# Kernel optimization log

Measured on AMD Instinct MI355X. Metric: run time of the kernel, lower is better.

The kernel has to match this reference:

```python
import jax, jax.numpy as jnp
import numpy as np

N_NODES = 30000
N_EDGES = 300000
N_TRIP = 200000
NUM_RELS = 8
F_RAW = 128
D = 256  # rgcn_in_dim == h_dim


def setup_inputs() -> dict:
    key = jax.random.key(0)
    ks = jax.random.split(key, 14)
    feats = jax.random.normal(ks[0], (N_NODES, F_RAW), jnp.float32)
    src = jax.random.randint(ks[1], (N_EDGES,), 0, N_NODES)
    dst = jax.random.randint(ks[2], (N_EDGES,), 0, N_NODES)
    etype = jax.random.randint(ks[3], (N_EDGES,), 0, NUM_RELS)
    trip_s = jax.random.randint(ks[4], (N_TRIP,), 0, N_NODES)
    trip_r = jax.random.randint(ks[5], (N_TRIP,), 0, NUM_RELS)
    trip_o = jax.random.randint(ks[6], (N_TRIP,), 0, N_NODES)
    # learned parameters
    W_affine = jax.random.normal(ks[7], (F_RAW, D), jnp.float32) * (1.0 / np.sqrt(F_RAW))
    b_affine = jnp.zeros((D,), jnp.float32)
    W_fwd = jax.random.normal(ks[8], (NUM_RELS, D, D), jnp.float32) * (1.0 / np.sqrt(D))
    W_bwd = jax.random.normal(ks[9], (NUM_RELS, D, D), jnp.float32) * (1.0 / np.sqrt(D))
    W_loop = jax.random.normal(ks[10], (D, D), jnp.float32) * (1.0 / np.sqrt(D))
    w_relation = jax.random.normal(ks[11], (NUM_RELS, D), jnp.float32)  # nn.init.normal_(0,1)
    return {
        "feats": feats, "W_affine": W_affine, "b_affine": b_affine,
        "W_fwd": W_fwd, "W_bwd": W_bwd, "W_loop": W_loop,
        "w_relation": w_relation,
        "src": src, "dst": dst, "etype": etype,
        "trip_s": trip_s, "trip_r": trip_r, "trip_o": trip_o,
    }


def reference(feats, W_affine, b_affine, W_fwd, W_bwd, W_loop, w_relation,
              src, dst, etype, trip_s, trip_r, trip_o):
    # LinearAffine: raw features -> rgcn_in_dim
    x = feats @ W_affine + b_affine                      # [N, D]
    n = x.shape[0]
    # Per-relation transforms of all node features: [R, N, D]
    tf = jnp.einsum('ni,rio->rno', x, W_fwd)
    tb = jnp.einsum('ni,rio->rno', x, W_bwd)
    # Forward-direction messages: gather per-edge transformed src, scatter-add to dst
    msg_f = tf[etype, src]                               # [E, D]
    agg = jnp.zeros((n, x.shape[1]), x.dtype).at[dst].add(msg_f)
    # Backward-direction messages: transformed dst features scattered to src
    msg_b = tb[etype, dst]                               # [E, D]
    agg = agg.at[src].add(msg_b)
    # Self-loop
    h = agg + x @ W_loop                                 # [N, D]
    # DistMult triplet scoring
    s = h[trip_s]
    r = w_relation[trip_r]
    o = h[trip_o]
    weights = jnp.sum(s * r * o, axis=1)                 # [T]
    return weights, h
```

## Files before the change

### kernel.cpp

```cpp
#include <hip/hip_runtime.h>

#define N_NODES 30000
#define N_EDGES 300000
#define N_TRIP 200000
#define NUM_RELS 8
#define F_RAW 128
#define DDIM 256

#define NBUCK (2 * NUM_RELS * N_NODES)
#define SCAN_CHUNK 1024
#define NCHUNK ((NBUCK + SCAN_CHUNK - 1) / SCAN_CHUNK)
#define NPAD (NCHUNK * SCAN_CHUNK)

#define KBIG 2304
#define KBWD 2048

typedef __attribute__((ext_vector_type(8))) short short8;
typedef __attribute__((ext_vector_type(8))) unsigned short u16x8;
typedef __attribute__((ext_vector_type(4))) float f32x4;

__device__ inline unsigned short f2bf(float f) {
  unsigned u = __builtin_bit_cast(unsigned, f);
  u = (u + 0x7FFFu + ((u >> 16) & 1u)) >> 16;
  return (unsigned short)u;
}
__device__ inline float bf2f(unsigned short s) {
  unsigned u = ((unsigned)s) << 16;
  return __builtin_bit_cast(float, u);
}

__global__ void zero_int_kernel(int* __restrict__ p, int n) {
  int i = blockIdx.x * blockDim.x + threadIdx.x;
  if (i < n) p[i] = 0;
}

__global__ void hist_kernel(const int* __restrict__ src,
                            const int* __restrict__ dst,
                            const int* __restrict__ et, int* __restrict__ cnt) {
  int e = blockIdx.x * blockDim.x + threadIdx.x;
  if (e >= N_EDGES) return;
  int r = et[e];
  atomicAdd(&cnt[r * N_NODES + dst[e]], 1);
  atomicAdd(&cnt[(NUM_RELS + r) * N_NODES + src[e]], 1);
}

__global__ __launch_bounds__(256) void scan1_kernel(const int* __restrict__ cnt,
                                                    int* __restrict__ offs,
                                                    int* __restrict__ bsum) {
  __shared__ int s[256];
  const int b = blockIdx.x, t = threadIdx.x;
  const int base = b * SCAN_CHUNK + t * 4;
  int4 v = *reinterpret_cast<const int4*>(&cnt[base]);
  int tsum = v.x + v.y + v.z + v.w;
  s[t] = tsum;
  __syncthreads();
  for (int off = 1; off < 256; off <<= 1) {
    int x = (t >= off) ? s[t - off] : 0;
    __syncthreads();
    s[t] += x;
    __syncthreads();
  }
  int excl = s[t] - tsum;
  offs[base + 0] = excl;
  offs[base + 1] = excl + v.x;
  offs[base + 2] = excl + v.x + v.y;
  offs[base + 3] = excl + v.x + v.y + v.z;
  if (t == 0) bsum[b] = s[255];
}

__global__ __launch_bounds__(512) void scan2_kernel(int* __restrict__ bsum) {
  __shared__ int s[512];
  const int t = threadIdx.x;
  int v = (t < NCHUNK) ? bsum[t] : 0;
  s[t] = v;
  __syncthreads();
  for (int off = 1; off < 512; off <<= 1) {
    int x = (t >= off) ? s[t - off] : 0;
    __syncthreads();
    s[t] += x;
    __syncthreads();
  }
  if (t < NCHUNK) bsum[t] = s[t] - v;
}

__global__ void scan3_kernel(int* __restrict__ offs,
                             const int* __restrict__ bsum,
                             int* __restrict__ cur) {
  int i = blockIdx.x * blockDim.x + threadIdx.x;
  if (i >= NPAD) return;
  int v = offs[i] + bsum[i / SCAN_CHUNK];
  offs[i] = v;
  if (i < NBUCK) cur[i] = v;
}

__global__ void fill_kernel(const int* __restrict__ src,
                            const int* __restrict__ dst,
                            const int* __restrict__ et, int* __restrict__ cur,
                            int* __restrict__ gidx) {
  int e = blockIdx.x * blockDim.x + threadIdx.x;
  if (e >= N_EDGES) return;
  int r = et[e];
  int s = src[e], d = dst[e];
  int p1 = atomicAdd(&cur[r * N_NODES + d], 1);
  gidx[p1] = s;
  int p2 = atomicAdd(&cur[(NUM_RELS + r) * N_NODES + s], 1);
  gidx[p2] = d;
}

__global__ void convert_bf16_kernel(const float* __restrict__ src,
                                    unsigned short* __restrict__ dst,
                                    int total) {
  const int i = blockIdx.x * blockDim.x + threadIdx.x;
  if (i < total) dst[i] = f2bf(src[i]);
}

__global__ void transpose_bf16_kernel(const float* __restrict__ src,
                                      unsigned short* __restrict__ dst,
                                      int R, int K, int N) {
  const int i = blockIdx.x * blockDim.x + threadIdx.x;
  const int total = R * K * N;
  if (i >= total) return;
  const int r = i / (K * N);
  const int rem = i - r * K * N;
  const int k = rem / N;
  const int n = rem - k * N;
  dst[(size_t)r * K * N + (size_t)n * K + k] = f2bf(src[i]);
}

__global__ void build_wcat2_kernel(const float* __restrict__ W8,
                                   const float* __restrict__ Wextra,
                                   unsigned short* __restrict__ dst, int KK) {
  const int i = blockIdx.x * blockDim.x + threadIdx.x;
  if (i >= 256 * KK) return;
  const int n = i / KK;
  const int kk = i - n * KK;
  float v;
  if (kk < 2048) {
    const int r = kk >> 8, k = kk & 255;
    v = W8[((size_t)r * 256 + k) * 256 + n];
  } else {
    v = Wextra[(size_t)(kk - 2048) * 256 + n];
  }
  dst[i] = f2bf(v);
}

__global__ __launch_bounds__(256) void gemm128_kernel(
    const unsigned short* __restrict__ A, int lda, int K,
    const unsigned short* __restrict__ Bt, const float* __restrict__ bias,
    unsigned short* __restrict__ Cb, int ldc, int M) {
  __shared__ __align__(16) unsigned short As[128 * 64];
  __shared__ __align__(16) unsigned short Bs[128 * 64];

  const int tid = threadIdx.x;
  const int lane = tid & 63;
  const int wave = tid >> 6;
  const int bm = blockIdx.y * 128;
  const int bn = blockIdx.x * 128;
  const int wr = wave >> 1;
  const int wc = wave & 1;
  const int g = lane >> 4;
  const int rl = lane & 15;

  f32x4 acc[4][4];
#pragma unroll
  for (int i = 0; i < 4; ++i)
#pragma unroll
    for (int j = 0; j < 4; ++j) acc[i][j] = (f32x4){0.f, 0.f, 0.f, 0.f};

  for (int k0 = 0; k0 < K; k0 += 64) {
#pragma unroll
    for (int c = 0; c < 8; ++c) {
      const int chunk = c * 4 + wave;
      if (chunk < 16) {
        const int S = chunk * 64 + lane;
        const int row = S >> 3;
        const int s = S & 7;
        int grow = bm + row;
        if (grow > M - 1) grow = M - 1;
        const int kcol = k0 + ((s ^ (row & 7)) << 3);
        const unsigned short* gp = A + (size_t)grow * lda + kcol;
        unsigned short* lp = As + (size_t)chunk * 512;
        __builtin_amdgcn_global_load_lds(
            (const __attribute__((address_space(1))) void*)gp,
            (__attribute__((address_space(3))) void*)lp, 16, 0, 0);
      } else {
        const int S = (chunk - 16) * 64 + lane;
        const int row = S >> 3;
        const int s = S & 7;
        const int kcol = k0 + ((s ^ (row & 7)) << 3);
        const unsigned short* gp = Bt + (size_t)(bn + row) * K + kcol;
        unsigned short* lp = Bs + (size_t)(chunk - 16) * 512;
        __builtin_amdgcn_global_load_lds(
            (const __attribute__((address_space(1))) void*)gp,
            (__attribute__((address_space(3))) void*)lp, 16, 0, 0);
      }
    }
    __syncthreads();

#pragma unroll
    for (int kk = 0; kk < 2; ++kk) {
      short8 a[4], b[4];
#pragma unroll
      for (int mi = 0; mi < 4; ++mi) {
        const int row = wr * 64 + mi * 16 + rl;
        const int slot = (kk * 4 + g) ^ (row & 7);
        a[mi] = *(const short8*)&As[row * 64 + slot * 8];
      }
#pragma unroll
      for (int ni = 0; ni < 4; ++ni) {
        const int row = wc * 64 + ni * 16 + rl;
        const int slot = (kk * 4 + g) ^ (row & 7);
        b[ni] = *(const short8*)&Bs[row * 64 + slot * 8];
      }
#pragma unroll
      for (int mi = 0; mi < 4; ++mi)
#pragma unroll
        for (int ni = 0; ni < 4; ++ni)
          acc[mi][ni] = __builtin_amdgcn_mfma_f32_16x16x32_bf16(
              a[mi], b[ni], acc[mi][ni], 0, 0, 0);
    }
    __syncthreads();
  }

#pragma unroll
  for (int mi = 0; mi < 4; ++mi) {
#pragma unroll
    for (int j = 0; j < 4; ++j) {
      const int row = bm + wr * 64 + mi * 16 + g * 4 + j;
      if (row >= M) continue;
#pragma unroll
      for (int ni = 0; ni < 4; ++ni) {
        const int col = bn + wc * 64 + ni * 16 + rl;
        Cb[(size_t)row * ldc + col] = f2bf(acc[mi][ni][j] + bias[col]);
      }
    }
  }
}

template <int OUT_MODE>
__global__ __launch_bounds__(256) void gemm64_kernel(
    const unsigned short* __restrict__ A, int lda, int K,
    const unsigned short* __restrict__ Bt, float* __restrict__ Cf,
    unsigned short* __restrict__ Cb, int ldc, int M, int nblk) {
  __shared__ __align__(16) unsigned short As[64 * 64];
  __shared__ __align__(16) unsigned short Bs[128 * 64];

  const int tid = threadIdx.x;
  const int lane = tid & 63;
  const int wave = tid >> 6;

  const int orig = blockIdx.x;
  const int q = nblk >> 3, r = nblk & 7;
  const int xcd = orig & 7, off = orig >> 3;
  const int wg =
      (xcd < r) ? xcd * (q + 1) + off : r * (q + 1) + (xcd - r) * q + off;
  const int bm = (wg >> 1) * 64;
  const int bn = (wg & 1) * 128;

  const int wr = wave >> 1;
  const int wc = wave & 1;
  const int g = lane >> 4;
  const int rl = lane & 15;

  f32x4 acc[2][4];
#pragma unroll
  for (int i = 0; i < 2; ++i)
#pragma unroll
    for (int j = 0; j < 4; ++j) acc[i][j] = (f32x4){0.f, 0.f, 0.f, 0.f};

  for (int k0 = 0; k0 < K; k0 += 64) {
#pragma unroll
    for (int c = 0; c < 6; ++c) {
      const int chunk = c * 4 + wave;
      if (chunk < 8) {
        const int S = chunk * 64 + lane;
        const int row = S >> 3;
        const int s = S & 7;
        int grow = bm + row;
        if (grow > M - 1) grow = M - 1;
        const unsigned short* gp =
            A + (size_t)grow * lda + k0 + ((s ^ (row & 7)) << 3);
        unsigned short* lp = As + (size_t)chunk * 512;
        __builtin_amdgcn_global_load_lds(
            (const __attribute__((address_space(1))) void*)gp,
            (__attribute__((address_space(3))) void*)lp, 16, 0, 0);
      } else {
        const int S = (chunk - 8) * 64 + lane;
        const int row = S >> 3;
        const int s = S & 7;
        const unsigned short* gp =
            Bt + (size_t)(bn + row) * K + k0 + ((s ^ (row & 7)) << 3);
        unsigned short* lp = Bs + (size_t)(chunk - 8) * 512;
        __builtin_amdgcn_global_load_lds(
            (const __attribute__((address_space(1))) void*)gp,
            (__attribute__((address_space(3))) void*)lp, 16, 0, 0);
      }
    }
    __syncthreads();

#pragma unroll
    for (int kk = 0; kk < 2; ++kk) {
      short8 a[2], b[4];
#pragma unroll
      for (int mi = 0; mi < 2; ++mi) {
        const int row = wr * 32 + mi * 16 + rl;
        const int slot = (kk * 4 + g) ^ (row & 7);
        a[mi] = *(const short8*)&As[row * 64 + slot * 8];
      }
#pragma unroll
      for (int ni = 0; ni < 4; ++ni) {
        const int row = wc * 64 + ni * 16 + rl;
        const int slot = (kk * 4 + g) ^ (row & 7);
        b[ni] = *(const short8*)&Bs[row * 64 + slot * 8];
      }
#pragma unroll
      for (int mi = 0; mi < 2; ++mi)
#pragma unroll
        for (int ni = 0; ni < 4; ++ni)
          acc[mi][ni] = __builtin_amdgcn_mfma_f32_16x16x32_bf16(
              a[mi], b[ni], acc[mi][ni], 0, 0, 0);
    }
    __syncthreads();
  }

#pragma unroll
  for (int mi = 0; mi < 2; ++mi) {
#pragma unroll
    for (int j = 0; j < 4; ++j) {
      const int row = bm + wr * 32 + mi * 16 + g * 4 + j;
      if (row >= M) continue;
#pragma unroll
      for (int ni = 0; ni < 4; ++ni) {
        const int col = bn + wc * 64 + ni * 16 + rl;
        float v = acc[mi][ni][j];
        const size_t idx = (size_t)row * ldc + col;
        if (OUT_MODE == 0) {
          Cf[idx] = v;
        } else {
          v += Cf[idx];
          Cf[idx] = v;
          Cb[idx] = f2bf(v);
        }
      }
    }
  }
}

__global__ __launch_bounds__(256) void zgatherw_kernel(
    unsigned short* __restrict__ Z, int colbase,
    const int* __restrict__ offs_base, const int* __restrict__ gidx) {
  const int lane = threadIdx.x & 63;
  const int hl = lane >> 5;
  const int l5 = lane & 31;
  const int b = blockIdx.x * 8 + (threadIdx.x >> 6) * 2 + hl;
  if (b >= NUM_RELS * N_NODES) return;
  const int r = b / N_NODES;
  const int v = b - r * N_NODES;
  const int s = offs_base[b], e = offs_base[b + 1];

  float acc[8] = {};
  for (int i = s; i < e; i += 4) {
    int g4[4];
    u16x8 xs[4];
#pragma unroll
    for (int q = 0; q < 4; ++q)
      if (i + q < e) g4[q] = gidx[i + q];
#pragma unroll
    for (int q = 0; q < 4; ++q)
      if (i + q < e)
        xs[q] = *(const u16x8*)&Z[(size_t)g4[q] * KBIG + 2048 + l5 * 8];
#pragma unroll
    for (int q = 0; q < 4; ++q)
      if (i + q < e) {
#pragma unroll
        for (int j = 0; j < 8; ++j) acc[j] += bf2f((unsigned short)xs[q][j]);
      }
  }
  u16x8 o;
#pragma unroll
  for (int j = 0; j < 8; ++j) o[j] = (short)f2bf(acc[j]);
  *(u16x8*)&Z[(size_t)v * KBIG + colbase + r * 256 + l5 * 8] = o;
}

__global__ __launch_bounds__(256) void score32_kernel(
    const unsigned short* __restrict__ hb, const float* __restrict__ wrel,
    const int* __restrict__ ts, const int* __restrict__ tr,
    const int* __restrict__ to, float* __restrict__ out, int T) {
  const int t = blockIdx.x * 8 + (threadIdx.x >> 5);
  if (t >= T) return;
  const int l5 = threadIdx.x & 31;
  const int s = ts[t];
  const int r = tr[t];
  const int o = to[t];
  const u16x8 hs = *(const u16x8*)&hb[(size_t)s * DDIM + l5 * 8];
  const u16x8 ho = *(const u16x8*)&hb[(size_t)o * DDIM + l5 * 8];
  const float4 w0 = *(const float4*)&wrel[(size_t)r * DDIM + l5 * 8];
  const float4 w1 = *(const float4*)&wrel[(size_t)r * DDIM + l5 * 8 + 4];
  float sum = bf2f((unsigned short)hs[0]) * w0.x * bf2f((unsigned short)ho[0]) +
              bf2f((unsigned short)hs[1]) * w0.y * bf2f((unsigned short)ho[1]) +
              bf2f((unsigned short)hs[2]) * w0.z * bf2f((unsigned short)ho[2]) +
              bf2f((unsigned short)hs[3]) * w0.w * bf2f((unsigned short)ho[3]) +
              bf2f((unsigned short)hs[4]) * w1.x * bf2f((unsigned short)ho[4]) +
              bf2f((unsigned short)hs[5]) * w1.y * bf2f((unsigned short)ho[5]) +
              bf2f((unsigned short)hs[6]) * w1.z * bf2f((unsigned short)ho[6]) +
              bf2f((unsigned short)hs[7]) * w1.w * bf2f((unsigned short)ho[7]);
#pragma unroll
  for (int off = 16; off; off >>= 1) sum += __shfl_down(sum, off, 32);
  if (l5 == 0) out[t] = sum;
}

extern "C" void kernel_launch(void* const* d_in, const int* in_sizes, int n_in,
                              void* d_out, int out_size, void* d_ws,
                              size_t ws_size, hipStream_t stream) {
  const float* feats = (const float*)d_in[0];
  const float* W_affine = (const float*)d_in[1];
  const float* b_affine = (const float*)d_in[2];
  const float* W_fwd = (const float*)d_in[3];
  const float* W_bwd = (const float*)d_in[4];
  const float* W_loop = (const float*)d_in[5];
  const float* w_relation = (const float*)d_in[6];
  const int* src = (const int*)d_in[7];
  const int* dst = (const int*)d_in[8];
  const int* etype = (const int*)d_in[9];
  const int* trip_s = (const int*)d_in[10];
  const int* trip_r = (const int*)d_in[11];
  const int* trip_o = (const int*)d_in[12];

  float* out_w = (float*)d_out;
  float* h = out_w + N_TRIP;

  char* ws = (char*)d_ws;
  unsigned short* fb = (unsigned short*)(ws);
  unsigned short* Z = (unsigned short*)(ws + 7680000);
  unsigned short* hbf = (unsigned short*)(ws + 145920000);
  unsigned short* Wta = (unsigned short*)(ws + 161280000);
  unsigned short* Wcat1 = (unsigned short*)(ws + 161345536);
  unsigned short* Wcat2 = (unsigned short*)(ws + 162525184);
  int* cnt = (int*)(ws + 163573760);
  int* offs = (int*)(ws + 165494784);
  int* cur = (int*)(ws + 167415808);
  int* bsum = (int*)(ws + 169336832);
  int* gidx = (int*)(ws + 169338880);

  zero_int_kernel<<<(NPAD + 255) / 256, 256, 0, stream>>>(cnt, NPAD);
  hist_kernel<<<(N_EDGES + 255) / 256, 256, 0, stream>>>(src, dst, etype, cnt);
  scan1_kernel<<<NCHUNK, 256, 0, stream>>>(cnt, offs, bsum);
  scan2_kernel<<<1, 512, 0, stream>>>(bsum);
  scan3_kernel<<<(NPAD + 255) / 256, 256, 0, stream>>>(offs, bsum, cur);
  fill_kernel<<<(N_EDGES + 255) / 256, 256, 0, stream>>>(src, dst, etype, cur,
                                                         gidx);

  convert_bf16_kernel<<<(N_NODES * F_RAW + 255) / 256, 256, 0, stream>>>(
      feats, fb, N_NODES * F_RAW);
  transpose_bf16_kernel<<<(F_RAW * DDIM + 255) / 256, 256, 0, stream>>>(
      W_affine, Wta, 1, F_RAW, DDIM);
  build_wcat2_kernel<<<(256 * KBIG + 255) / 256, 256, 0, stream>>>(
      W_fwd, W_loop, Wcat1, KBIG);
  build_wcat2_kernel<<<(256 * KBWD + 255) / 256, 256, 0, stream>>>(
      W_bwd, nullptr, Wcat2, KBWD);

  const dim3 agrid(2, (N_NODES + 127) / 128);
  gemm128_kernel<<<agrid, 256, 0, stream>>>(fb, F_RAW, F_RAW, Wta, b_affine,
                                            Z + 2048, KBIG, N_NODES);

  const int nblk = 2 * ((N_NODES + 63) / 64);
  const int zgrid = (NUM_RELS * N_NODES + 7) / 8;

  zgatherw_kernel<<<zgrid, 256, 0, stream>>>(Z, 0, offs, gidx);
  gemm64_kernel<0><<<nblk, 256, 0, stream>>>(Z, KBIG, KBIG, Wcat1, h, nullptr,
                                             DDIM, N_NODES, nblk);
  zgatherw_kernel<<<zgrid, 256, 0, stream>>>(Z, 0, offs + NUM_RELS * N_NODES,
                                             gidx);
  gemm64_kernel<2><<<nblk, 256, 0, stream>>>(Z, KBIG, KBWD, Wcat2, h, hbf,
                                             DDIM, N_NODES, nblk);

  score32_kernel<<<(N_TRIP + 7) / 8, 256, 0, stream>>>(
      hbf, w_relation, trip_s, trip_r, trip_o, out_w, N_TRIP);
}
```

Before: 298.1 us.

## Merge fwd/bwd GEMMs into one K=4352 pass with indirect sparse row pointers

Replaces the two dense Z-buffer gathers and two GEMMs with a single gather that only materialises bucket sums for buckets with two or more edges. Empty buckets point to a shared zero row and single-edge buckets point straight at the node's x row. One GEMM over the concatenated forward, backward and loop weights then reads A rows through a rowptr indirection. This removes the large dense Z writes and the read-modify-write of h between the two GEMMs. In exchange it adds a rowptr pass with an atomic slot counter and per-load indirect addressing in the GEMM A tile loads.

```diff
diff --git a/kernel.cpp b/kernel.cpp
--- a/kernel.cpp
+++ b/kernel.cpp
@@ -12,8 +12,10 @@
 #define NCHUNK ((NBUCK + SCAN_CHUNK - 1) / SCAN_CHUNK)
 #define NPAD (NCHUNK * SCAN_CHUNK)
 
-#define KBIG 2304
-#define KBWD 2048
+#define KMRG 4352
+#define ZM_ROWS 240000
+#define XB_ROW0 240000
+#define ZERO_ROW 270000
 
 typedef __attribute__((ext_vector_type(8))) short short8;
 typedef __attribute__((ext_vector_type(8))) unsigned short u16x8;
@@ -85,8 +87,11 @@
 
 __global__ void scan3_kernel(int* __restrict__ offs,
                              const int* __restrict__ bsum,
-                             int* __restrict__ cur) {
+                             int* __restrict__ cur, int* __restrict__ zrow,
+                             int* __restrict__ ctr) {
   int i = blockIdx.x * blockDim.x + threadIdx.x;
+  if (i < 128) zrow[i] = 0;
+  if (i == 0) *ctr = 0;
   if (i >= NPAD) return;
   int v = offs[i] + bsum[i / SCAN_CHUNK];
   offs[i] = v;
@@ -107,6 +112,24 @@
   gidx[p2] = d;
 }
 
+__global__ void rowptr_kernel(const int* __restrict__ offs,
+                              const int* __restrict__ gidx,
+                              int* __restrict__ rowptr, int* __restrict__ ctr) {
+  int b = blockIdx.x * blockDim.x + threadIdx.x;
+  if (b >= NBUCK) return;
+  int s = offs[b], e = offs[b + 1];
+  int cnt = e - s;
+  int rid;
+  if (cnt == 0) rid = ZERO_ROW;
+  else if (cnt == 1) rid = XB_ROW0 + gidx[s];
+  else {
+    int slot = atomicAdd(ctr, 1);
+    if (slot > ZM_ROWS - 1) slot = ZM_ROWS - 1;
+    rid = slot;
+  }
+  rowptr[b] = rid;
+}
+
 __global__ void convert_bf16_kernel(const float* __restrict__ src,
                                     unsigned short* __restrict__ dst,
                                     int total) {
@@ -127,19 +150,23 @@
   dst[(size_t)r * K * N + (size_t)n * K + k] = f2bf(src[i]);
 }
 
-__global__ void build_wcat2_kernel(const float* __restrict__ W8,
-                                   const float* __restrict__ Wextra,
-                                   unsigned short* __restrict__ dst, int KK) {
+__global__ void build_wcat3_kernel(const float* __restrict__ Wf,
+                                   const float* __restrict__ Wb,
+                                   const float* __restrict__ Wl,
+                                   unsigned short* __restrict__ dst) {
   const int i = blockIdx.x * blockDim.x + threadIdx.x;
-  if (i >= 256 * KK) return;
-  const int n = i / KK;
-  const int kk = i - n * KK;
+  if (i >= 256 * KMRG) return;
+  const int n = i / KMRG;
+  const int kk = i - n * KMRG;
   float v;
   if (kk < 2048) {
     const int r = kk >> 8, k = kk & 255;
-    v = W8[((size_t)r * 256 + k) * 256 + n];
+    v = Wf[((size_t)r * 256 + k) * 256 + n];
+  } else if (kk < 4096) {
+    const int r = (kk - 2048) >> 8, k = kk & 255;
+    v = Wb[((size_t)r * 256 + k) * 256 + n];
   } else {
-    v = Wextra[(size_t)(kk - 2048) * 256 + n];
+    v = Wl[(size_t)(kk - 4096) * 256 + n];
   }
   dst[i] = f2bf(v);
 }
@@ -237,11 +264,46 @@
   }
 }
 
-template <int OUT_MODE>
-__global__ __launch_bounds__(256) void gemm64_kernel(
-    const unsigned short* __restrict__ A, int lda, int K,
-    const unsigned short* __restrict__ Bt, float* __restrict__ Cf,
-    unsigned short* __restrict__ Cb, int ldc, int M, int nblk) {
+__global__ __launch_bounds__(256) void zgatherm_kernel(
+    unsigned short* __restrict__ rowbase, const unsigned short* __restrict__ xb,
+    const int* __restrict__ offs, const int* __restrict__ gidx,
+    const int* __restrict__ rowptr) {
+  const int lane = threadIdx.x & 63;
+  const int hl = lane >> 5;
+  const int l5 = lane & 31;
+  const int b = blockIdx.x * 8 + (threadIdx.x >> 6) * 2 + hl;
+  if (b >= NBUCK) return;
+  const int s = offs[b], e = offs[b + 1];
+  if (e - s < 2) return;
+
+  float acc[8] = {};
+  for (int i = s; i < e; i += 4) {
+    int g4[4];
+    u16x8 xs[4];
+#pragma unroll
+    for (int q = 0; q < 4; ++q)
+      if (i + q < e) g4[q] = gidx[i + q];
+#pragma unroll
+    for (int q = 0; q < 4; ++q)
+      if (i + q < e)
+        xs[q] = *(const u16x8*)&xb[(size_t)g4[q] * DDIM + l5 * 8];
+#pragma unroll
+    for (int q = 0; q < 4; ++q)
+      if (i + q < e) {
+#pragma unroll
+        for (int j = 0; j < 8; ++j) acc[j] += bf2f((unsigned short)xs[q][j]);
+      }
+  }
+  u16x8 o;
+#pragma unroll
+  for (int j = 0; j < 8; ++j) o[j] = (short)f2bf(acc[j]);
+  *(u16x8*)&rowbase[(size_t)rowptr[b] * DDIM + l5 * 8] = o;
+}
+
+__global__ __launch_bounds__(256) void gemmv_kernel(
+    const unsigned short* __restrict__ rowbase,
+    const int* __restrict__ rowptr, const unsigned short* __restrict__ Bt,
+    float* __restrict__ Cf, unsigned short* __restrict__ Cb, int M, int nblk) {
   __shared__ __align__(16) unsigned short As[64 * 64];
   __shared__ __align__(16) unsigned short Bs[128 * 64];
 
@@ -268,7 +330,9 @@
 #pragma unroll
     for (int j = 0; j < 4; ++j) acc[i][j] = (f32x4){0.f, 0.f, 0.f, 0.f};
 
-  for (int k0 = 0; k0 < K; k0 += 64) {
+  for (int k0 = 0; k0 < KMRG; k0 += 64) {
+    const int kb = k0 >> 8;
+    const int koff = k0 & 255;
 #pragma unroll
     for (int c = 0; c < 6; ++c) {
       const int chunk = c * 4 + wave;
@@ -276,10 +340,12 @@
         const int S = chunk * 64 + lane;
         const int row = S >> 3;
         const int s = S & 7;
-        int grow = bm + row;
-        if (grow > M - 1) grow = M - 1;
+        int node = bm + row;
+        if (node > M - 1) node = M - 1;
+        const int rid =
+            (kb < 16) ? rowptr[kb * N_NODES + node] : (XB_ROW0 + node);
         const unsigned short* gp =
-            A + (size_t)grow * lda + k0 + ((s ^ (row & 7)) << 3);
+            rowbase + (size_t)rid * 256 + koff + ((s ^ (row & 7)) << 3);
         unsigned short* lp = As + (size_t)chunk * 512;
         __builtin_amdgcn_global_load_lds(
             (const __attribute__((address_space(1))) void*)gp,
@@ -289,7 +355,7 @@
         const int row = S >> 3;
         const int s = S & 7;
         const unsigned short* gp =
-            Bt + (size_t)(bn + row) * K + k0 + ((s ^ (row & 7)) << 3);
+            Bt + (size_t)(bn + row) * KMRG + k0 + ((s ^ (row & 7)) << 3);
         unsigned short* lp = Bs + (size_t)(chunk - 8) * 512;
         __builtin_amdgcn_global_load_lds(
             (const __attribute__((address_space(1))) void*)gp,
@@ -332,54 +398,13 @@
 #pragma unroll
       for (int ni = 0; ni < 4; ++ni) {
         const int col = bn + wc * 64 + ni * 16 + rl;
-        float v = acc[mi][ni][j];
-        const size_t idx = (size_t)row * ldc + col;
-        if (OUT_MODE == 0) {
-          Cf[idx] = v;
-        } else {
-          v += Cf[idx];
-          Cf[idx] = v;
-          Cb[idx] = f2bf(v);
-        }
+        const float v = acc[mi][ni][j];
+        const size_t idx = (size_t)row * DDIM + col;
+        Cf[idx] = v;
+        Cb[idx] = f2bf(v);
       }
     }
   }
-}
-
-__global__ __launch_bounds__(256) void zgatherw_kernel(
-    unsigned short* __restrict__ Z, int colbase,
-    const int* __restrict__ offs_base, const int* __restrict__ gidx) {
-  const int lane = threadIdx.x & 63;
-  const int hl = lane >> 5;
-  const int l5 = lane & 31;
-  const int b = blockIdx.x * 8 + (threadIdx.x >> 6) * 2 + hl;
-  if (b >= NUM_RELS * N_NODES) return;
-  const int r = b / N_NODES;
-  const int v = b - r * N_NODES;
-  const int s = offs_base[b], e = offs_base[b + 1];
-
-  float acc[8] = {};
-  for (int i = s; i < e; i += 4) {
-    int g4[4];
-    u16x8 xs[4];
-#pragma unroll
-    for (int q = 0; q < 4; ++q)
-      if (i + q < e) g4[q] = gidx[i + q];
-#pragma unroll
-    for (int q = 0; q < 4; ++q)
-      if (i + q < e)
-        xs[q] = *(const u16x8*)&Z[(size_t)g4[q] * KBIG + 2048 + l5 * 8];
-#pragma unroll
-    for (int q = 0; q < 4; ++q)
-      if (i + q < e) {
-#pragma unroll
-        for (int j = 0; j < 8; ++j) acc[j] += bf2f((unsigned short)xs[q][j]);
-      }
-  }
-  u16x8 o;
-#pragma unroll
-  for (int j = 0; j < 8; ++j) o[j] = (short)f2bf(acc[j]);
-  *(u16x8*)&Z[(size_t)v * KBIG + colbase + r * 256 + l5 * 8] = o;
 }
 
 __global__ __launch_bounds__(256) void score32_kernel(
@@ -430,49 +455,49 @@
   float* h = out_w + N_TRIP;
 
   char* ws = (char*)d_ws;
-  unsigned short* fb = (unsigned short*)(ws);
-  unsigned short* Z = (unsigned short*)(ws + 7680000);
-  unsigned short* hbf = (unsigned short*)(ws + 145920000);
-  unsigned short* Wta = (unsigned short*)(ws + 161280000);
-  unsigned short* Wcat1 = (unsigned short*)(ws + 161345536);
-  unsigned short* Wcat2 = (unsigned short*)(ws + 162525184);
-  int* cnt = (int*)(ws + 163573760);
-  int* offs = (int*)(ws + 165494784);
-  int* cur = (int*)(ws + 167415808);
-  int* bsum = (int*)(ws + 169336832);
-  int* gidx = (int*)(ws + 169338880);
-
-  zero_int_kernel<<<(NPAD + 255) / 256, 256, 0, stream>>>(cnt, NPAD);
-  hist_kernel<<<(N_EDGES + 255) / 256, 256, 0, stream>>>(src, dst, etype, cnt);
-  scan1_kernel<<<NCHUNK, 256, 0, stream>>>(cnt, offs, bsum);
+  unsigned short* rowbase = (unsigned short*)ws;
+  unsigned short* fb = (unsigned short*)ws;
+  unsigned short* xb = (unsigned short*)(ws + 122880000);
+  int* zrow = (int*)(ws + 138240000);
+  unsigned short* hbf = (unsigned short*)(ws + 138240512);
+  int* offs = (int*)(ws + 153600512);
+  int* cntcur = (int*)(ws + 155522048);
+  int* bsum = (int*)(ws + 157443072);
+  int* gidx = (int*)(ws + 157445120);
+  int* rowptr = (int*)(ws + 159845120);
+  unsigned short* Wta = (unsigned short*)(ws + 161765120);
+  unsigned short* Wcat = (unsigned short*)(ws + 161830656);
+  int* ctr = (int*)(ws + 164058880);
+
+  zero_int_kernel<<<(NPAD + 255) / 256, 256, 0, stream>>>(cntcur, NPAD);
+  hist_kernel<<<(N_EDGES + 255) / 256, 256, 0, stream>>>(src, dst, etype,
+                                                         cntcur);
+  scan1_kernel<<<NCHUNK, 256, 0, stream>>>(cntcur, offs, bsum);
   scan2_kernel<<<1, 512, 0, stream>>>(bsum);
-  scan3_kernel<<<(NPAD + 255) / 256, 256, 0, stream>>>(offs, bsum, cur);
-  fill_kernel<<<(N_EDGES + 255) / 256, 256, 0, stream>>>(src, dst, etype, cur,
-                                                         gidx);
+  scan3_kernel<<<(NPAD + 255) / 256, 256, 0, stream>>>(offs, bsum, cntcur,
+                                                       zrow, ctr);
+  fill_kernel<<<(N_EDGES + 255) / 256, 256, 0, stream>>>(src, dst, etype,
+                                                         cntcur, gidx);
+  rowptr_kernel<<<(NBUCK + 255) / 256, 256, 0, stream>>>(offs, gidx, rowptr,
+                                                         ctr);
 
   convert_bf16_kernel<<<(N_NODES * F_RAW + 255) / 256, 256, 0, stream>>>(
       feats, fb, N_NODES * F_RAW);
   transpose_bf16_kernel<<<(F_RAW * DDIM + 255) / 256, 256, 0, stream>>>(
       W_affine, Wta, 1, F_RAW, DDIM);
-  build_wcat2_kernel<<<(256 * KBIG + 255) / 256, 256, 0, stream>>>(
-      W_fwd, W_loop, Wcat1, KBIG);
-  build_wcat2_kernel<<<(256 * KBWD + 255) / 256, 256, 0, stream>>>(
-      W_bwd, nullptr, Wcat2, KBWD);
+  build_wcat3_kernel<<<(256 * KMRG + 255) / 256, 256, 0, stream>>>(
+      W_fwd, W_bwd, W_loop, Wcat);
 
   const dim3 agrid(2, (N_NODES + 127) / 128);
   gemm128_kernel<<<agrid, 256, 0, stream>>>(fb, F_RAW, F_RAW, Wta, b_affine,
-                                            Z + 2048, KBIG, N_NODES);
+                                            xb, DDIM, N_NODES);
+
+  zgatherm_kernel<<<(NBUCK + 7) / 8, 256, 0, stream>>>(rowbase, xb, offs, gidx,
+                                                       rowptr);
 
   const int nblk = 2 * ((N_NODES + 63) / 64);
-  const int zgrid = (NUM_RELS * N_NODES + 7) / 8;
-
-  zgatherw_kernel<<<zgrid, 256, 0, stream>>>(Z, 0, offs, gidx);
-  gemm64_kernel<0><<<nblk, 256, 0, stream>>>(Z, KBIG, KBIG, Wcat1, h, nullptr,
-                                             DDIM, N_NODES, nblk);
-  zgatherw_kernel<<<zgrid, 256, 0, stream>>>(Z, 0, offs + NUM_RELS * N_NODES,
-                                             gidx);
-  gemm64_kernel<2><<<nblk, 256, 0, stream>>>(Z, KBIG, KBWD, Wcat2, h, hbf,
-                                             DDIM, N_NODES, nblk);
+  gemmv_kernel<<<nblk, 256, 0, stream>>>(rowbase, rowptr, Wcat, h, hbf,
+                                         N_NODES, nblk);
 
   score32_kernel<<<(N_TRIP + 7) / 8, 256, 0, stream>>>(
       hbf, w_relation, trip_s, trip_r, trip_o, out_w, N_TRIP);
```

Result: slower. 379.8 us (+27.4%).

## Split-K the relation GEMMs in two with atomic float accumulation

Applied to the files above, without the earlier changes.

Each 64x128 output tile of the two large relation GEMMs is now computed by two blocks, each covering half of K, and both add their partial sums into the fp32 output with atomicAdd. This doubles the grid so more CUs are busy. In exchange it needs a kernel to zero h beforehand and a separate pass to convert h to bf16, and the atomic traffic plus the extra passes add memory work. It also makes the float summation order nondeterministic.

```diff
diff --git a/kernel.cpp b/kernel.cpp
--- a/kernel.cpp
+++ b/kernel.cpp
@@ -32,6 +32,11 @@
 __global__ void zero_int_kernel(int* __restrict__ p, int n) {
   int i = blockIdx.x * blockDim.x + threadIdx.x;
   if (i < n) p[i] = 0;
+}
+
+__global__ void zero4_kernel(float* __restrict__ p, int n4) {
+  int i = blockIdx.x * blockDim.x + threadIdx.x;
+  if (i < n4) *(f32x4*)&p[i * 4] = (f32x4){0.f, 0.f, 0.f, 0.f};
 }
 
 __global__ void hist_kernel(const int* __restrict__ src,
@@ -237,11 +242,10 @@
   }
 }
 
-template <int OUT_MODE>
-__global__ __launch_bounds__(256) void gemm64_kernel(
+__global__ __launch_bounds__(256) void gemm64a_kernel(
     const unsigned short* __restrict__ A, int lda, int K,
-    const unsigned short* __restrict__ Bt, float* __restrict__ Cf,
-    unsigned short* __restrict__ Cb, int ldc, int M, int nblk) {
+    const unsigned short* __restrict__ Bt, float* __restrict__ Cf, int M,
+    int nblk) {
   __shared__ __align__(16) unsigned short As[64 * 64];
   __shared__ __align__(16) unsigned short Bs[128 * 64];
 
@@ -254,8 +258,11 @@
   const int xcd = orig & 7, off = orig >> 3;
   const int wg =
       (xcd < r) ? xcd * (q + 1) + off : r * (q + 1) + (xcd - r) * q + off;
-  const int bm = (wg >> 1) * 64;
-  const int bn = (wg & 1) * 128;
+  const int bm = (wg >> 2) * 64;
+  const int bn = ((wg >> 1) & 1) * 128;
+  const int kseg = wg & 1;
+  const int khalf = K >> 1;
+  const int klo = kseg * khalf;
 
   const int wr = wave >> 1;
   const int wc = wave & 1;
@@ -268,7 +275,7 @@
 #pragma unroll
     for (int j = 0; j < 4; ++j) acc[i][j] = (f32x4){0.f, 0.f, 0.f, 0.f};
 
-  for (int k0 = 0; k0 < K; k0 += 64) {
+  for (int k0 = klo; k0 < klo + khalf; k0 += 64) {
 #pragma unroll
     for (int c = 0; c < 6; ++c) {
       const int chunk = c * 4 + wave;
@@ -332,18 +339,24 @@
 #pragma unroll
       for (int ni = 0; ni < 4; ++ni) {
         const int col = bn + wc * 64 + ni * 16 + rl;
-        float v = acc[mi][ni][j];
-        const size_t idx = (size_t)row * ldc + col;
-        if (OUT_MODE == 0) {
-          Cf[idx] = v;
-        } else {
-          v += Cf[idx];
-          Cf[idx] = v;
-          Cb[idx] = f2bf(v);
-        }
-      }
-    }
-  }
+        atomicAdd(&Cf[(size_t)row * DDIM + col], acc[mi][ni][j]);
+      }
+    }
+  }
+}
+
+__global__ void h2bf_kernel(const float* __restrict__ h,
+                            unsigned short* __restrict__ hbf, int n8) {
+  const int i = blockIdx.x * blockDim.x + threadIdx.x;
+  if (i >= n8) return;
+  const f32x4 lo = *(const f32x4*)&h[i * 8];
+  const f32x4 hi = *(const f32x4*)&h[i * 8 + 4];
+  u16x8 o;
+#pragma unroll
+  for (int j = 0; j < 4; ++j) o[j] = f2bf(lo[j]);
+#pragma unroll
+  for (int j = 0; j < 4; ++j) o[4 + j] = f2bf(hi[j]);
+  *(u16x8*)&hbf[i * 8] = o;
 }
 
 __global__ __launch_bounds__(256) void zgatherw_kernel(
@@ -458,21 +471,26 @@
       W_fwd, W_loop, Wcat1, KBIG);
   build_wcat2_kernel<<<(256 * KBWD + 255) / 256, 256, 0, stream>>>(
       W_bwd, nullptr, Wcat2, KBWD);
+  zero4_kernel<<<(N_NODES * DDIM / 4 + 255) / 256, 256, 0, stream>>>(
+      h, N_NODES * DDIM / 4);
 
   const dim3 agrid(2, (N_NODES + 127) / 128);
   gemm128_kernel<<<agrid, 256, 0, stream>>>(fb, F_RAW, F_RAW, Wta, b_affine,
                                             Z + 2048, KBIG, N_NODES);
 
-  const int nblk = 2 * ((N_NODES + 63) / 64);
+  const int nblk = 4 * ((N_NODES + 63) / 64);
   const int zgrid = (NUM_RELS * N_NODES + 7) / 8;
 
   zgatherw_kernel<<<zgrid, 256, 0, stream>>>(Z, 0, offs, gidx);
-  gemm64_kernel<0><<<nblk, 256, 0, stream>>>(Z, KBIG, KBIG, Wcat1, h, nullptr,
-                                             DDIM, N_NODES, nblk);
+  gemm64a_kernel<<<nblk, 256, 0, stream>>>(Z, KBIG, KBIG, Wcat1, h, N_NODES,
+                                           nblk);
   zgatherw_kernel<<<zgrid, 256, 0, stream>>>(Z, 0, offs + NUM_RELS * N_NODES,
                                              gidx);
-  gemm64_kernel<2><<<nblk, 256, 0, stream>>>(Z, KBIG, KBWD, Wcat2, h, hbf,
-                                             DDIM, N_NODES, nblk);
+  gemm64a_kernel<<<nblk, 256, 0, stream>>>(Z, KBIG, KBWD, Wcat2, h, N_NODES,
+                                           nblk);
+
+  h2bf_kernel<<<(N_NODES * DDIM / 8 + 255) / 256, 256, 0, stream>>>(
+      h, hbf, N_NODES * DDIM / 8);
 
   score32_kernel<<<(N_TRIP + 7) / 8, 256, 0, stream>>>(
       hbf, w_relation, trip_s, trip_r, trip_o, out_w, N_TRIP);
```

Result: slower. 368.5 us (+23.6%).
